# Optimization experiments

Hardware: AMD Instinct MI355X
Metric: run time of the kernel (lower is better)

Reference implementation:

```python
import jax, jax.numpy as jnp
import numpy as np

N_NODES = 20000
N_EDGES = 200000
D_IN, D_H1, D_H2, D_OUT = 1433, 1000, 500, 7


def setup_inputs() -> dict:
    key = jax.random.key(0)
    ks = jax.random.split(key, 8)
    features = jax.random.normal(ks[0], (N_NODES, D_IN), dtype=jnp.float32)
    src = jax.random.randint(ks[1], (N_EDGES,), 0, N_NODES)
    dst = jax.random.randint(ks[2], (N_EDGES,), 0, N_NODES)
    W1 = jax.random.normal(ks[3], (D_IN, D_H1), dtype=jnp.float32) * 0.02
    b1 = jnp.zeros((D_H1,), dtype=jnp.float32)
    W2 = jax.random.normal(ks[4], (D_H1, D_H2), dtype=jnp.float32) * 0.02
    b2 = jnp.zeros((D_H2,), dtype=jnp.float32)
    W3 = jax.random.normal(ks[5], (D_H2, D_OUT), dtype=jnp.float32) * 0.02
    b3 = jnp.zeros((D_OUT,), dtype=jnp.float32)
    return {"features": features, "src": src, "dst": dst,
            "W1": W1, "b1": b1, "W2": W2, "b2": b2, "W3": W3, "b3": b3}


def reference(features, src, dst, W1, b1, W2, b2, W3, b3):
    N = features.shape[0]

    def agg(x):  # sum_tensors over incoming neighbors: h_i = sum_{(j->i) in E} x_j
        return jax.ops.segment_sum(x[src], dst, num_segments=N)

    # GCN layer 1: aggregate -> linear -> relu
    x = jax.nn.relu(agg(features) @ W1 + b1)       # [N, 1000]
    # GCN layer 2: aggregate -> linear -> relu (dropout = identity in eval)
    x = jax.nn.relu(agg(x) @ W2 + b2)              # [N, 500]
    # output linear -> relu (dropout = identity in eval)
    x = jax.nn.relu(x @ W3 + b3)                   # [N, 7]
    return x
```

## Files before the change

kernel.cpp:

```cpp
#include <hip/hip_runtime.h>
#include <hip/hip_bf16.h>


#define N_NODES 20000
#define N_EDGES 200000
#define D_IN    1433
#define D_H1    1000
#define D_H2    500
#define D_OUT   7

#define MPAD    20096
#define K1PAD   1440
#define N1PAD   1024
#define K2PAD   1024
#define N2PAD   512
#define H1STR   1008
#define H2STR   504

typedef __attribute__((ext_vector_type(8))) short short8;
typedef __attribute__((ext_vector_type(8))) unsigned short ushort8_t;
typedef __attribute__((ext_vector_type(4))) float f32x4;

__device__ __forceinline__ unsigned short bf16_rne(float x) {
    unsigned int u = __float_as_uint(x);
    u = (u + 0x7FFFu + ((u >> 16) & 1u)) >> 16;
    return (unsigned short)u;
}
__device__ __forceinline__ float bf16_up(unsigned short h) {
    return __uint_as_float((unsigned int)h << 16);
}

__device__ __forceinline__ void gl_lds16(const unsigned short* g, unsigned short* lds) {
    __builtin_amdgcn_global_load_lds(
        (const __attribute__((address_space(1))) unsigned int*)g,
        (__attribute__((address_space(3))) unsigned int*)lds, 16, 0, 0);
}

__global__ __launch_bounds__(256) void count_deg(const int* __restrict__ dst,
                                                 int* __restrict__ offs) {
    int e = blockIdx.x * 256 + threadIdx.x;
    if (e < N_EDGES) atomicAdd(&offs[dst[e] + 1], 1);
}

__global__ __launch_bounds__(1024) void scan_inclusive(int* __restrict__ data, int n) {
    __shared__ int buf[1024];
    __shared__ int carry;
    int t = threadIdx.x;
    if (t == 0) carry = 0;
    __syncthreads();
    for (int base = 0; base < n; base += 1024) {
        int i = base + t;
        int v = (i < n) ? data[i] : 0;
        buf[t] = v;
        __syncthreads();
        #pragma unroll
        for (int s = 1; s < 1024; s <<= 1) {
            int u = (t >= s) ? buf[t - s] : 0;
            __syncthreads();
            buf[t] += u;
            __syncthreads();
        }
        int c = carry;
        if (i < n) data[i] = buf[t] + c;
        __syncthreads();
        if (t == 1023) carry = c + buf[1023];
        __syncthreads();
    }
}

__global__ __launch_bounds__(256) void fill_csr(const int* __restrict__ src,
                                                const int* __restrict__ dst,
                                                int* __restrict__ cursor,
                                                int* __restrict__ srcs) {
    int e = blockIdx.x * 256 + threadIdx.x;
    if (e < N_EDGES) {
        int pos = atomicAdd(&cursor[dst[e]], 1);
        srcs[pos] = src[e];
    }
}

__global__ __launch_bounds__(256) void cast_features(const float* __restrict__ F,
                                                     unsigned int* __restrict__ out) {
    int row = blockIdx.x;
    int t = threadIdx.x;
    const float* fr = F + (size_t)row * D_IN;
    bool live = row < N_NODES;
    for (int kk = t; kk < K1PAD / 2; kk += 256) {
        int k0 = kk * 2;
        float a = (live && k0     < D_IN) ? fr[k0]     : 0.f;
        float b = (live && k0 + 1 < D_IN) ? fr[k0 + 1] : 0.f;
        out[(size_t)row * (K1PAD / 2) + kk] =
            (unsigned int)bf16_rne(a) | ((unsigned int)bf16_rne(b) << 16);
    }
}

template <int SR, int SC, int DR, int DC>
__global__ __launch_bounds__(256) void transpose_cast_pad(const float* __restrict__ src,
                                                          unsigned short* __restrict__ dst) {
    __shared__ float tile[32][33];
    int c0 = blockIdx.x * 32;
    int r0 = blockIdx.y * 32;
    int tx = threadIdx.x & 31, ty = threadIdx.x >> 5;
    #pragma unroll
    for (int p = 0; p < 4; ++p) {
        int r = r0 + ty + p * 8, c = c0 + tx;
        tile[ty + p * 8][tx] = (r < SR && c < SC) ? src[(size_t)r * SC + c] : 0.f;
    }
    __syncthreads();
    #pragma unroll
    for (int p = 0; p < 4; ++p) {
        int dr = c0 + ty + p * 8;
        int dc = r0 + tx;
        if (dr < DR && dc < DC) dst[(size_t)dr * DC + dc] = bf16_rne(tile[tx][ty + p * 8]);
    }
}

template <int KPAD>
__global__ __launch_bounds__(256) void gemm_mfma(const unsigned short* __restrict__ A,
                                                 const unsigned short* __restrict__ B,
                                                 unsigned short* __restrict__ C,
                                                 int M, int N, int OSTR) {
    __shared__ __align__(16) unsigned short sA[128 * 32];
    __shared__ __align__(16) unsigned short sB[128 * 32];
    const int t = threadIdx.x;
    const int w = t >> 6, lane = t & 63;
    const int m0 = blockIdx.y * 128, n0 = blockIdx.x * 128;
    const int wm = (w >> 1) * 64, wn = (w & 1) * 64;

    const int srow = lane >> 2;
    const int skc  = (lane & 3) * 8;
    const int mrow = lane & 15, quad = lane >> 4;

    f32x4 acc[4][4] = {};

    for (int k0 = 0; k0 < KPAD; k0 += 32) {
        #pragma unroll
        for (int c = 0; c < 2; ++c) {
            int rbase = c * 64 + w * 16;
            gl_lds16(A + (size_t)(m0 + rbase + srow) * KPAD + k0 + skc, &sA[rbase * 32]);
            gl_lds16(B + (size_t)(n0 + rbase + srow) * KPAD + k0 + skc, &sB[rbase * 32]);
        }
        __syncthreads();

        short8 af[4], bf[4];
        #pragma unroll
        for (int mt = 0; mt < 4; ++mt)
            af[mt] = *(const short8*)&sA[(wm + mt * 16 + mrow) * 32 + quad * 8];
        #pragma unroll
        for (int nt = 0; nt < 4; ++nt)
            bf[nt] = *(const short8*)&sB[(wn + nt * 16 + mrow) * 32 + quad * 8];
        #pragma unroll
        for (int mt = 0; mt < 4; ++mt)
            #pragma unroll
            for (int nt = 0; nt < 4; ++nt)
                acc[mt][nt] = __builtin_amdgcn_mfma_f32_16x16x32_bf16(
                    af[mt], bf[nt], acc[mt][nt], 0, 0, 0);
        __syncthreads();
    }

    #pragma unroll
    for (int mt = 0; mt < 4; ++mt) {
        int m = m0 + wm + mt * 16 + quad * 4;
        #pragma unroll
        for (int nt = 0; nt < 4; ++nt) {
            int n = n0 + wn + nt * 16 + mrow;
            if (n >= N) continue;
            #pragma unroll
            for (int r = 0; r < 4; ++r)
                if (m + r < M) C[(size_t)(m + r) * OSTR + n] = bf16_rne(acc[mt][nt][r]);
        }
    }
}

__global__ __launch_bounds__(128) void agg1_bf16(const unsigned short* __restrict__ H,
                                                 const int* __restrict__ offs,
                                                 const int* __restrict__ srcs,
                                                 const float* __restrict__ bias,
                                                 unsigned short* __restrict__ X) {
    __shared__ int sl[128];
    const int i = blockIdx.x, t = threadIdx.x;
    const int beg = offs[i], end = offs[i + 1];
    const bool active = t < 125;
    float s[8] = {};
    for (int base = beg; base < end; base += 128) {
        int n = min(128, end - base);
        __syncthreads();
        if (t < n) sl[t] = srcs[base + t];
        __syncthreads();
        if (active) {
            for (int e = 0; e < n; ++e) {
                ushort8_t v = *(const ushort8_t*)(H + (size_t)sl[e] * H1STR + t * 8);
                #pragma unroll
                for (int u = 0; u < 8; ++u) s[u] += bf16_up(v[u]);
            }
        }
    }
    ushort8_t o = (ushort8_t)0;
    if (active) {
        #pragma unroll
        for (int u = 0; u < 8; ++u)
            o[u] = bf16_rne(fmaxf(s[u] + bias[t * 8 + u], 0.f));
    }
    *(ushort8_t*)(X + (size_t)i * K2PAD + t * 8) = o;
}

__global__ __launch_bounds__(128) void agg2_out(const unsigned short* __restrict__ H,
                                                const int* __restrict__ offs,
                                                const int* __restrict__ srcs,
                                                const float* __restrict__ b2,
                                                const float* __restrict__ W3,
                                                const float* __restrict__ b3,
                                                float* __restrict__ out) {
    __shared__ int sl[128];
    __shared__ float red[2][8];
    const int i = blockIdx.x, t = threadIdx.x;
    const int beg = offs[i], end = offs[i + 1];
    const bool active = t < 125;
    float s[4] = {};
    for (int base = beg; base < end; base += 128) {
        int n = min(128, end - base);
        __syncthreads();
        if (t < n) sl[t] = srcs[base + t];
        __syncthreads();
        if (active) {
            for (int e = 0; e < n; ++e) {
                ushort4 v = *(const ushort4*)(H + (size_t)sl[e] * H2STR + t * 4);
                s[0] += bf16_up(v.x); s[1] += bf16_up(v.y);
                s[2] += bf16_up(v.z); s[3] += bf16_up(v.w);
            }
        }
    }
    float acc[D_OUT] = {};
    if (active) {
        #pragma unroll
        for (int u = 0; u < 4; ++u) {
            float x = fmaxf(s[u] + b2[t * 4 + u], 0.f);
            const float* w = W3 + (size_t)(t * 4 + u) * D_OUT;
            #pragma unroll
            for (int j = 0; j < D_OUT; ++j) acc[j] += x * w[j];
        }
    }
    #pragma unroll
    for (int j = 0; j < D_OUT; ++j)
        #pragma unroll
        for (int off = 32; off; off >>= 1) acc[j] += __shfl_down(acc[j], off);
    const int lane = t & 63, wave = t >> 6;
    if (lane == 0) {
        #pragma unroll
        for (int j = 0; j < D_OUT; ++j) red[wave][j] = acc[j];
    }
    __syncthreads();
    if (t == 0) {
        #pragma unroll
        for (int j = 0; j < D_OUT; ++j)
            out[(size_t)i * D_OUT + j] = fmaxf(red[0][j] + red[1][j] + b3[j], 0.f);
    }
}

extern "C" void kernel_launch(void* const* d_in, const int* in_sizes, int n_in,
                              void* d_out, int out_size, void* d_ws, size_t ws_size,
                              hipStream_t stream) {
    const float* features = (const float*)d_in[0];
    const int*   src      = (const int*)d_in[1];
    const int*   dst      = (const int*)d_in[2];
    const float* W1       = (const float*)d_in[3];
    const float* b1       = (const float*)d_in[4];
    const float* W2       = (const float*)d_in[5];
    const float* b2       = (const float*)d_in[6];
    const float* W3       = (const float*)d_in[7];
    const float* b3       = (const float*)d_in[8];
    float* out = (float*)d_out;

    char* ws = (char*)d_ws;
    unsigned short* Fbf  = (unsigned short*)(ws + 0);
    unsigned short* X1bf = (unsigned short*)(ws + 0);
    unsigned short* H1   = (unsigned short*)(ws + 57876480);
    unsigned short* H2   = (unsigned short*)(ws + 57876480);
    unsigned short* W1T  = (unsigned short*)(ws + 98196480);
    unsigned short* W2T  = (unsigned short*)(ws + 101145600);
    int* offs   = (int*)(ws + 102194176);
    int* cursor = (int*)(ws + 102274304);
    int* srcs   = (int*)(ws + 102354432);

    hipMemsetAsync(offs, 0, (N_NODES + 1) * sizeof(int), stream);
    count_deg<<<(N_EDGES + 255) / 256, 256, 0, stream>>>(dst, offs);
    scan_inclusive<<<1, 1024, 0, stream>>>(offs, N_NODES + 1);
    hipMemcpyAsync(cursor, offs, N_NODES * sizeof(int), hipMemcpyDeviceToDevice, stream);
    fill_csr<<<(N_EDGES + 255) / 256, 256, 0, stream>>>(src, dst, cursor, srcs);

    cast_features<<<MPAD, 256, 0, stream>>>(features, (unsigned int*)Fbf);
    transpose_cast_pad<D_IN, D_H1, N1PAD, K1PAD>
        <<<dim3(N1PAD / 32, K1PAD / 32), 256, 0, stream>>>(W1, W1T);
    transpose_cast_pad<D_H1, D_H2, N2PAD, K2PAD>
        <<<dim3(N2PAD / 32, K2PAD / 32), 256, 0, stream>>>(W2, W2T);

    gemm_mfma<K1PAD><<<dim3(N1PAD / 128, MPAD / 128), 256, 0, stream>>>(
        Fbf, W1T, H1, N_NODES, D_H1, H1STR);
    hipMemsetAsync(ws + (size_t)N_NODES * K2PAD * 2, 0,
                   (size_t)(MPAD - N_NODES) * K2PAD * 2, stream);
    agg1_bf16<<<N_NODES, 128, 0, stream>>>(H1, offs, srcs, b1, X1bf);

    gemm_mfma<K2PAD><<<dim3(N2PAD / 128, MPAD / 128), 256, 0, stream>>>(
        X1bf, W2T, H2, N_NODES, D_H2, H2STR);
    agg2_out<<<N_NODES, 128, 0, stream>>>(H2, offs, srcs, b2, W3, b3, out);
}
```

Measured before the change: 494.1 us.

## Remap GEMM blocks per XCD, swizzle LDS, streamline scan and aggregation kernels

The GEMM grid becomes 1D and is remapped so that blocks sharing the same M-row tile land on the same XCD, which should improve L2 reuse. The LDS fill and read offsets are XOR-swizzled to reduce bank conflicts. The scan now uses wave shuffles instead of a barrier-heavy LDS scan and writes the cursor array directly, which removes a memcpy. The aggregation kernels drop LDS staging of neighbor indices, and agg1 now zero-fills the padding rows itself, which removes a memset launch.

```diff
diff --git a/kernel.cpp b/kernel.cpp
--- a/kernel.cpp
+++ b/kernel.cpp
@@ -16,6 +16,7 @@
 #define N2PAD   512
 #define H1STR   1008
 #define H2STR   504
+#define MBLK    157
 
 typedef __attribute__((ext_vector_type(8))) short short8;
 typedef __attribute__((ext_vector_type(8))) unsigned short ushort8_t;
@@ -42,29 +43,32 @@
     if (e < N_EDGES) atomicAdd(&offs[dst[e] + 1], 1);
 }
 
-__global__ __launch_bounds__(1024) void scan_inclusive(int* __restrict__ data, int n) {
-    __shared__ int buf[1024];
-    __shared__ int carry;
-    int t = threadIdx.x;
-    if (t == 0) carry = 0;
+__global__ __launch_bounds__(1024) void scan_csr(int* __restrict__ offs,
+                                                 int* __restrict__ cursor, int n) {
+    __shared__ int wsum[16];
+    __shared__ int s_carry;
+    const int t = threadIdx.x, lane = t & 63, wv = t >> 6;
+    if (t == 0) s_carry = 0;
     __syncthreads();
     for (int base = 0; base < n; base += 1024) {
         int i = base + t;
-        int v = (i < n) ? data[i] : 0;
-        buf[t] = v;
+        int v = (i < n) ? offs[i] : 0;
+        #pragma unroll
+        for (int s = 1; s < 64; s <<= 1) {
+            int u = __shfl_up(v, s, 64);
+            if (lane >= s) v += u;
+        }
+        if (lane == 63) wsum[wv] = v;
         __syncthreads();
-        #pragma unroll
-        for (int s = 1; s < 1024; s <<= 1) {
-            int u = (t >= s) ? buf[t - s] : 0;
-            __syncthreads();
-            buf[t] += u;
-            __syncthreads();
-        }
-        int c = carry;
-        if (i < n) data[i] = buf[t] + c;
+        int prefix = s_carry;
+        for (int k = 0; k < wv; ++k) prefix += wsum[k];
+        v += prefix;
+        if (i < n) {
+            offs[i] = v;
+            if (i < N_NODES) cursor[i] = v;
+        }
         __syncthreads();
-        if (t == 1023) carry = c + buf[1023];
-        __syncthreads();
+        if (t == 1023) s_carry = v;
     }
 }
 
@@ -115,21 +119,32 @@
     }
 }
 
-template <int KPAD>
+template <int KPAD, int NB>
 __global__ __launch_bounds__(256) void gemm_mfma(const unsigned short* __restrict__ A,
                                                  const unsigned short* __restrict__ B,
                                                  unsigned short* __restrict__ C,
                                                  int M, int N, int OSTR) {
     __shared__ __align__(16) unsigned short sA[128 * 32];
     __shared__ __align__(16) unsigned short sB[128 * 32];
+    const int bid = blockIdx.x;
+    const int xcd = bid & 7;
+    const int tt  = bid >> 3;
+    const int nb  = tt % NB;
+    const int mb  = (tt / NB) * 8 + xcd;
+    if (mb >= MBLK) return;
+
     const int t = threadIdx.x;
     const int w = t >> 6, lane = t & 63;
-    const int m0 = blockIdx.y * 128, n0 = blockIdx.x * 128;
+    const int m0 = mb * 128, n0 = nb * 128;
     const int wm = (w >> 1) * 64, wn = (w & 1) * 64;
 
     const int srow = lane >> 2;
-    const int skc  = (lane & 3) * 8;
+    const int skc  = ((lane & 3) ^ ((lane >> 3) & 3)) * 8;
     const int mrow = lane & 15, quad = lane >> 4;
+    const int rslot = ((quad ^ ((mrow >> 1) & 3)) & 3) * 8;
+
+    const unsigned short* Aptr = A + (size_t)(m0 + srow) * KPAD + skc;
+    const unsigned short* Bptr = B + (size_t)(n0 + srow) * KPAD + skc;
 
     f32x4 acc[4][4] = {};
 
@@ -137,18 +152,19 @@
         #pragma unroll
         for (int c = 0; c < 2; ++c) {
             int rbase = c * 64 + w * 16;
-            gl_lds16(A + (size_t)(m0 + rbase + srow) * KPAD + k0 + skc, &sA[rbase * 32]);
-            gl_lds16(B + (size_t)(n0 + rbase + srow) * KPAD + k0 + skc, &sB[rbase * 32]);
-        }
+            gl_lds16(Aptr + (size_t)rbase * KPAD, &sA[rbase * 32]);
+            gl_lds16(Bptr + (size_t)rbase * KPAD, &sB[rbase * 32]);
+        }
+        Aptr += 32; Bptr += 32;
         __syncthreads();
 
         short8 af[4], bf[4];
         #pragma unroll
         for (int mt = 0; mt < 4; ++mt)
-            af[mt] = *(const short8*)&sA[(wm + mt * 16 + mrow) * 32 + quad * 8];
+            af[mt] = *(const short8*)&sA[(wm + mt * 16 + mrow) * 32 + rslot];
         #pragma unroll
         for (int nt = 0; nt < 4; ++nt)
-            bf[nt] = *(const short8*)&sB[(wn + nt * 16 + mrow) * 32 + quad * 8];
+            bf[nt] = *(const short8*)&sB[(wn + nt * 16 + mrow) * 32 + rslot];
         #pragma unroll
         for (int mt = 0; mt < 4; ++mt)
             #pragma unroll
@@ -177,29 +193,24 @@
                                                  const int* __restrict__ srcs,
                                                  const float* __restrict__ bias,
                                                  unsigned short* __restrict__ X) {
-    __shared__ int sl[128];
     const int i = blockIdx.x, t = threadIdx.x;
-    const int beg = offs[i], end = offs[i + 1];
     const bool active = t < 125;
-    float s[8] = {};
-    for (int base = beg; base < end; base += 128) {
-        int n = min(128, end - base);
-        __syncthreads();
-        if (t < n) sl[t] = srcs[base + t];
-        __syncthreads();
+    const int tc = active ? t : 124;
+    ushort8_t o = (ushort8_t)0;
+    if (i < N_NODES) {
+        const int beg = offs[i], end = offs[i + 1];
+        float s[8] = {};
+        for (int e = beg; e < end; ++e) {
+            const int j = srcs[e];
+            ushort8_t v = *(const ushort8_t*)(H + (size_t)j * H1STR + tc * 8);
+            #pragma unroll
+            for (int u = 0; u < 8; ++u) s[u] += bf16_up(v[u]);
+        }
         if (active) {
-            for (int e = 0; e < n; ++e) {
-                ushort8_t v = *(const ushort8_t*)(H + (size_t)sl[e] * H1STR + t * 8);
-                #pragma unroll
-                for (int u = 0; u < 8; ++u) s[u] += bf16_up(v[u]);
-            }
-        }
-    }
-    ushort8_t o = (ushort8_t)0;
-    if (active) {
-        #pragma unroll
-        for (int u = 0; u < 8; ++u)
-            o[u] = bf16_rne(fmaxf(s[u] + bias[t * 8 + u], 0.f));
+            #pragma unroll
+            for (int u = 0; u < 8; ++u)
+                o[u] = bf16_rne(fmaxf(s[u] + bias[t * 8 + u], 0.f));
+        }
     }
     *(ushort8_t*)(X + (size_t)i * K2PAD + t * 8) = o;
 }
@@ -211,33 +222,26 @@
                                                 const float* __restrict__ W3,
                                                 const float* __restrict__ b3,
                                                 float* __restrict__ out) {
-    __shared__ int sl[128];
     __shared__ float red[2][8];
     const int i = blockIdx.x, t = threadIdx.x;
+    const bool active = t < 125;
+    const int tc = active ? t : 124;
     const int beg = offs[i], end = offs[i + 1];
-    const bool active = t < 125;
     float s[4] = {};
-    for (int base = beg; base < end; base += 128) {
-        int n = min(128, end - base);
-        __syncthreads();
-        if (t < n) sl[t] = srcs[base + t];
-        __syncthreads();
-        if (active) {
-            for (int e = 0; e < n; ++e) {
-                ushort4 v = *(const ushort4*)(H + (size_t)sl[e] * H2STR + t * 4);
-                s[0] += bf16_up(v.x); s[1] += bf16_up(v.y);
-                s[2] += bf16_up(v.z); s[3] += bf16_up(v.w);
-            }
-        }
+    for (int e = beg; e < end; ++e) {
+        const int j = srcs[e];
+        ushort4 v = *(const ushort4*)(H + (size_t)j * H2STR + tc * 4);
+        s[0] += bf16_up(v.x); s[1] += bf16_up(v.y);
+        s[2] += bf16_up(v.z); s[3] += bf16_up(v.w);
     }
     float acc[D_OUT] = {};
     if (active) {
         #pragma unroll
         for (int u = 0; u < 4; ++u) {
             float x = fmaxf(s[u] + b2[t * 4 + u], 0.f);
-            const float* w = W3 + (size_t)(t * 4 + u) * D_OUT;
-            #pragma unroll
-            for (int j = 0; j < D_OUT; ++j) acc[j] += x * w[j];
+            const float* wr = W3 + (size_t)(t * 4 + u) * D_OUT;
+            #pragma unroll
+            for (int j = 0; j < D_OUT; ++j) acc[j] += x * wr[j];
         }
     }
     #pragma unroll
@@ -284,8 +288,7 @@
 
     hipMemsetAsync(offs, 0, (N_NODES + 1) * sizeof(int), stream);
     count_deg<<<(N_EDGES + 255) / 256, 256, 0, stream>>>(dst, offs);
-    scan_inclusive<<<1, 1024, 0, stream>>>(offs, N_NODES + 1);
-    hipMemcpyAsync(cursor, offs, N_NODES * sizeof(int), hipMemcpyDeviceToDevice, stream);
+    scan_csr<<<1, 1024, 0, stream>>>(offs, cursor, N_NODES + 1);
     fill_csr<<<(N_EDGES + 255) / 256, 256, 0, stream>>>(src, dst, cursor, srcs);
 
     cast_features<<<MPAD, 256, 0, stream>>>(features, (unsigned int*)Fbf);
@@ -294,13 +297,11 @@
     transpose_cast_pad<D_H1, D_H2, N2PAD, K2PAD>
         <<<dim3(N2PAD / 32, K2PAD / 32), 256, 0, stream>>>(W2, W2T);
 
-    gemm_mfma<K1PAD><<<dim3(N1PAD / 128, MPAD / 128), 256, 0, stream>>>(
+    gemm_mfma<K1PAD, N1PAD / 128><<<8 * (N1PAD / 128) * 20, 256, 0, stream>>>(
         Fbf, W1T, H1, N_NODES, D_H1, H1STR);
-    hipMemsetAsync(ws + (size_t)N_NODES * K2PAD * 2, 0,
-                   (size_t)(MPAD - N_NODES) * K2PAD * 2, stream);
-    agg1_bf16<<<N_NODES, 128, 0, stream>>>(H1, offs, srcs, b1, X1bf);
-
-    gemm_mfma<K2PAD><<<dim3(N2PAD / 128, MPAD / 128), 256, 0, stream>>>(
+    agg1_bf16<<<MPAD, 128, 0, stream>>>(H1, offs, srcs, b1, X1bf);
+
+    gemm_mfma<K2PAD, N2PAD / 128><<<8 * (N2PAD / 128) * 20, 256, 0, stream>>>(
         X1bf, W2T, H2, N_NODES, D_H2, H2STR);
     agg2_out<<<N_NODES, 128, 0, stream>>>(H2, offs, srcs, b2, W3, b3, out);
 }
```

Measured after the change: 457.5 us. 1.08x faster.
